# Optimization experiments

Measured on AMD Instinct MI355X. Metric: run time of the kernel, lower is better.

The kernel has to match this reference:

```python
import jax, jax.numpy as jnp
import numpy as np

B = 1_000_000   # reflections
K = 16_384      # groups
E = 64          # encoder_out
H = 64          # hidden_dim


def setup_inputs() -> dict:
    key = jax.random.key(0)
    ks = jax.random.split(key, 12)
    x = jax.random.normal(ks[0], (B, E), dtype=jnp.float32)
    gl = jax.random.randint(ks[1], (B,), 0, K)
    # guarantee every group id 0..K-1 appears, so torch.unique == arange(K)
    gl = gl.at[:K].set(jnp.arange(K))
    s = 0.05
    W1 = jax.random.normal(ks[2], (E, H), jnp.float32) * s
    b1 = jax.random.normal(ks[3], (H,), jnp.float32) * s
    W2 = jax.random.normal(ks[4], (H, H), jnp.float32) * s
    b2 = jax.random.normal(ks[5], (H,), jnp.float32) * s
    W3 = jax.random.normal(ks[6], (H, H), jnp.float32) * s
    b3 = jax.random.normal(ks[7], (H,), jnp.float32) * s
    w_mu = jax.random.normal(ks[8], (H, 1), jnp.float32) * s
    b_mu = jnp.full((1,), -6.9, jnp.float32)   # log_tau_init
    w_lv = jax.random.normal(ks[9], (H, 1), jnp.float32) * s
    b_lv = jnp.full((1,), -2.0, jnp.float32)
    return {"x": x, "group_labels": gl, "W1": W1, "b1": b1, "W2": W2, "b2": b2,
            "W3": W3, "b3": b3, "w_mu": w_mu, "b_mu": b_mu, "w_lv": w_lv, "b_lv": b_lv}


def reference(x, group_labels, W1, b1, W2, b2, W3, b3, w_mu, b_mu, w_lv, b_lv):
    # phi: Linear -> SiLU -> Linear -> SiLU
    z = jax.nn.silu(jax.nn.silu(x @ W1 + b1) @ W2 + b2)          # (B, H)
    # segment mean by group (math-equivalent to the dense one-hot matmul)
    counts = jax.ops.segment_sum(jnp.ones((z.shape[0],), z.dtype),
                                 group_labels, num_segments=K)    # (K,)
    gsum = jax.ops.segment_sum(z, group_labels, num_segments=K)   # (K, H)
    group_features = gsum / counts[:, None]
    # rho + heads
    h = jax.nn.silu(group_features @ W3 + b3)                     # (K, H)
    mu = (h @ w_mu + b_mu)[:, 0]                                  # (K,)
    logvar = jnp.clip((h @ w_lv + b_lv)[:, 0], -10.0, 4.0)        # (K,)
    std = jnp.exp(0.5 * logvar)
    eps = jax.random.normal(jax.random.key(42), std.shape, std.dtype)
    log_tau = mu + std * eps                                      # reparam sample
    tau_group = jnp.exp(log_tau)
    # unique_groups == arange(K) by construction -> searchsorted is identity
    tau_per_refl = tau_group[group_labels][:, None]               # (B, 1)
    log_tau_per_refl = log_tau[group_labels][:, None]             # (B, 1)
    return (mu, logvar, tau_per_refl, log_tau_per_refl)
```

## Files before the change

### kernel.cpp

```cpp
#include <hip/hip_runtime.h>

#define BN 1000000
#define KN 16384
#define HN 64
#define TPB 384
#define NW  6

typedef __bf16 bf16x8 __attribute__((ext_vector_type(8)));
typedef float  f32x4  __attribute__((ext_vector_type(4)));
typedef unsigned short u16x8 __attribute__((ext_vector_type(8)));

__device__ __forceinline__ unsigned short f2bf(float f) {
    unsigned u = __float_as_uint(f);
    u += 0x7fffu + ((u >> 16) & 1u);
    return (unsigned short)(u >> 16);
}
__device__ __forceinline__ float bf2f(unsigned short b) {
    return __uint_as_float(((unsigned)b) << 16);
}
__device__ __forceinline__ float silu_f(float v) {
    return v * __builtin_amdgcn_rcpf(1.0f + __expf(-v));
}
__device__ __forceinline__ f32x4 mfma16(bf16x8 a, bf16x8 b, f32x4 c) {
    return __builtin_amdgcn_mfma_f32_16x16x32_bf16(a, b, c, 0, 0, 0);
}

__device__ __forceinline__ float erfinv_xla(float x) {
    float w = -log1pf(-x * x);
    float p;
    if (w < 5.0f) {
        w -= 2.5f;
        p = 2.81022636e-08f;
        p = fmaf(p, w, 3.43273939e-07f);
        p = fmaf(p, w, -3.5233877e-06f);
        p = fmaf(p, w, -4.39150654e-06f);
        p = fmaf(p, w, 0.00021858087f);
        p = fmaf(p, w, -0.00125372503f);
        p = fmaf(p, w, -0.00417768164f);
        p = fmaf(p, w, 0.246640727f);
        p = fmaf(p, w, 1.50140941f);
    } else {
        w = sqrtf(w) - 3.0f;
        p = -0.000200214257f;
        p = fmaf(p, w, 0.000100950558f);
        p = fmaf(p, w, 0.00134934322f);
        p = fmaf(p, w, -0.00367342844f);
        p = fmaf(p, w, 0.00573950773f);
        p = fmaf(p, w, -0.0076224613f);
        p = fmaf(p, w, 0.00943887047f);
        p = fmaf(p, w, 1.00167406f);
        p = fmaf(p, w, 2.83297682f);
    }
    return p * x;
}

__device__ __forceinline__ float jax_eps16384(int gid) {
    const unsigned k0 = 0u, k1 = 42u, k2 = 0x1BD11BDAu ^ 0u ^ 42u;
    unsigned x0 = 0u + k0;
    unsigned x1 = (unsigned)gid + k1;
#define TF_RND(r) { x0 += x1; x1 = (x1 << (r)) | (x1 >> (32 - (r))); x1 ^= x0; }
    TF_RND(13) TF_RND(15) TF_RND(26) TF_RND(6)  x0 += k1; x1 += k2 + 1u;
    TF_RND(17) TF_RND(29) TF_RND(16) TF_RND(24) x0 += k2; x1 += k0 + 2u;
    TF_RND(13) TF_RND(15) TF_RND(26) TF_RND(6)  x0 += k0; x1 += k1 + 3u;
    TF_RND(17) TF_RND(29) TF_RND(16) TF_RND(24) x0 += k1; x1 += k2 + 4u;
    TF_RND(13) TF_RND(15) TF_RND(26) TF_RND(6)  x0 += k2; x1 += k0 + 5u;
#undef TF_RND
    unsigned bits = x0 ^ x1;
    float f = __uint_as_float((bits >> 9) | 0x3f800000u) - 1.0f;
    const float mn = -0.99999994f;
    float u = fmaxf(f * 2.0f + mn, mn);
    return 1.41421354f * erfinv_xla(u);
}

__global__ __launch_bounds__(256) void k_count(const int* __restrict__ gl,
                                               int* __restrict__ counts,
                                               float4* __restrict__ gz) {
    int i = blockIdx.x * 256 + threadIdx.x;
    const float4 z4 = make_float4(0.f, 0.f, 0.f, 0.f);
    for (int j = i; j < KN * HN / 4; j += 250112) gz[j] = z4;
    if (i < BN / 4) {
        int4 g = ((const int4*)gl)[i];
        atomicAdd(&counts[g.x], 1); atomicAdd(&counts[g.y], 1);
        atomicAdd(&counts[g.z], 1); atomicAdd(&counts[g.w], 1);
    }
}

__global__ __launch_bounds__(1024) void k_scan(const int* __restrict__ counts, int* __restrict__ cursor) {
    __shared__ int wtot[16];
    const int t = threadIdx.x, lane = t & 63, wv = t >> 6;
    const int4* c4 = (const int4*)counts;
    int4 q0 = c4[t * 4], q1 = c4[t * 4 + 1], q2 = c4[t * 4 + 2], q3 = c4[t * 4 + 3];
    int c[16] = {q0.x, q0.y, q0.z, q0.w, q1.x, q1.y, q1.z, q1.w,
                 q2.x, q2.y, q2.z, q2.w, q3.x, q3.y, q3.z, q3.w};
    int loc[16], s = 0;
    #pragma unroll
    for (int i = 0; i < 16; ++i) { loc[i] = s; s += c[i]; }
    const int own = s;
    #pragma unroll
    for (int off = 1; off < 64; off <<= 1) {
        int v = __shfl_up(s, off);
        if (lane >= off) s += v;
    }
    if (lane == 63) wtot[wv] = s;
    __syncthreads();
    int wbase = 0;
    #pragma unroll
    for (int w = 0; w < 16; ++w) wbase += (w < wv) ? wtot[w] : 0;
    const int ebase = wbase + s - own;
    int o[16];
    #pragma unroll
    for (int i = 0; i < 16; ++i) o[i] = ebase + loc[i];
    int4* o4 = (int4*)cursor;
    o4[t * 4]     = make_int4(o[0],  o[1],  o[2],  o[3]);
    o4[t * 4 + 1] = make_int4(o[4],  o[5],  o[6],  o[7]);
    o4[t * 4 + 2] = make_int4(o[8],  o[9],  o[10], o[11]);
    o4[t * 4 + 3] = make_int4(o[12], o[13], o[14], o[15]);
}

__global__ __launch_bounds__(256) void k_scatter(const int* __restrict__ gl, int* __restrict__ cursor,
                                                 int2* __restrict__ spk) {
    int i = blockIdx.x * 256 + threadIdx.x;
    if (i < BN / 4) {
        int4 g = ((const int4*)gl)[i];
        int r = i * 4;
        int p0 = atomicAdd(&cursor[g.x], 1); spk[p0] = make_int2(r,     g.x);
        int p1 = atomicAdd(&cursor[g.y], 1); spk[p1] = make_int2(r + 1, g.y);
        int p2 = atomicAdd(&cursor[g.z], 1); spk[p2] = make_int2(r + 2, g.z);
        int p3 = atomicAdd(&cursor[g.w], 1); spk[p3] = make_int2(r + 3, g.w);
    }
}

__global__ __launch_bounds__(TPB, 3) void k_phase1(
    const float* __restrict__ x, const int2* __restrict__ spk,
    const float* __restrict__ W1, const float* __restrict__ b1,
    const float* __restrict__ W2, const float* __restrict__ b2,
    float* __restrict__ gsum)
{
    __shared__ __align__(16) unsigned short w1t[64 * 64];
    __shared__ __align__(16) unsigned short w2t[64 * 64];
    __shared__ __align__(16) unsigned short xh[NW][64 * 64];
    __shared__ float b1s[64], b2s[64];
    __shared__ __align__(16) int sg_s[TPB];

    const int t = threadIdx.x;
    const int wv = t >> 6, lane = t & 63;
    const int lj = lane & 15, lg = lane >> 4;
    const int base  = blockIdx.x * TPB;
    const int wbase = base + wv * 64;

    const float4* W1v = (const float4*)W1;
    const float4* W2v = (const float4*)W2;
    float4 wa[3], wb[3];
    #pragma unroll
    for (int i = 0; i < 3; ++i) {
        int e4 = i * TPB + t;
        if (e4 < 1024) { wa[i] = W1v[e4]; wb[i] = W2v[e4]; }
    }

    int rid[4];
    #pragma unroll
    for (int rt = 0; rt < 4; ++rt) {
        int r = wbase + rt * 16 + lj;
        rid[rt] = (r < BN) ? spk[r].x : 0;
    }
    float4 xr[4][4];
    #pragma unroll
    for (int rt = 0; rt < 4; ++rt) {
        const float* xp = x + (size_t)rid[rt] * 64 + lg * 8;
        xr[rt][0] = *(const float4*)(xp);
        xr[rt][1] = *(const float4*)(xp + 4);
        xr[rt][2] = *(const float4*)(xp + 32);
        xr[rt][3] = *(const float4*)(xp + 36);
    }

    #pragma unroll
    for (int i = 0; i < 3; ++i) {
        int e4 = i * TPB + t;
        if (e4 < 1024) {
            int k  = e4 >> 4;
            int j0 = (e4 & 15) * 4;
            float av[4] = {wa[i].x, wa[i].y, wa[i].z, wa[i].w};
            float bv[4] = {wb[i].x, wb[i].y, wb[i].z, wb[i].w};
            #pragma unroll
            for (int c = 0; c < 4; ++c) {
                int j = j0 + c;
                int off = j * 128 + ((2 * k) ^ ((j & 7) << 4));
                *(unsigned short*)((char*)w1t + off) = f2bf(av[c]);
                *(unsigned short*)((char*)w2t + off) = f2bf(bv[c]);
            }
        }
    }
    if (t < 64) { b1s[t] = b1[t]; b2s[t] = b2[t]; }
    sg_s[t] = (base + t < BN) ? spk[base + t].y : -1;
    __syncthreads();

    bf16x8 af[4][2];
    #pragma unroll
    for (int rt = 0; rt < 4; ++rt)
        #pragma unroll
        for (int kk = 0; kk < 2; ++kk) {
            float4 a = xr[rt][kk * 2], b = xr[rt][kk * 2 + 1];
            u16x8 u;
            u[0] = f2bf(a.x); u[1] = f2bf(a.y); u[2] = f2bf(a.z); u[3] = f2bf(a.w);
            u[4] = f2bf(b.x); u[5] = f2bf(b.y); u[6] = f2bf(b.z); u[7] = f2bf(b.w);
            af[rt][kk] = __builtin_bit_cast(bf16x8, u);
        }

    unsigned short* myx = &xh[wv][0];

    f32x4 acc[4][4];
    #pragma unroll
    for (int a = 0; a < 4; ++a)
        #pragma unroll
        for (int b = 0; b < 4; ++b) acc[a][b] = f32x4{0.f, 0.f, 0.f, 0.f};

    #pragma unroll
    for (int kk = 0; kk < 2; ++kk) {
        const int kbyte = kk * 64 + lg * 16;
        bf16x8 bw[4];
        #pragma unroll
        for (int ct = 0; ct < 4; ++ct) {
            int row = ct * 16 + lj;
            bw[ct] = *(const bf16x8*)((char*)w1t + row * 128 + (kbyte ^ ((row & 7) << 4)));
        }
        #pragma unroll
        for (int rt = 0; rt < 4; ++rt)
            #pragma unroll
            for (int ct = 0; ct < 4; ++ct)
                acc[rt][ct] = mfma16(af[rt][kk], bw[ct], acc[rt][ct]);
    }
    {
        float bc[4];
        #pragma unroll
        for (int ct = 0; ct < 4; ++ct) bc[ct] = b1s[ct * 16 + lj];
        #pragma unroll
        for (int rt = 0; rt < 4; ++rt) {
            #pragma unroll
            for (int ct = 0; ct < 4; ++ct) {
                f32x4 v = acc[rt][ct];
                #pragma unroll
                for (int rg = 0; rg < 4; ++rg) {
                    int row = rt * 16 + lg * 4 + rg;
                    int col = ct * 16 + lj;
                    float h = silu_f(v[rg] + bc[ct]);
                    int off = row * 128 + ((2 * col) ^ ((row & 7) << 4));
                    *(unsigned short*)((char*)myx + off) = f2bf(h);
                }
                acc[rt][ct] = f32x4{0.f, 0.f, 0.f, 0.f};
            }
        }
    }

    #pragma unroll
    for (int kk = 0; kk < 2; ++kk) {
        const int kbyte = kk * 64 + lg * 16;
        bf16x8 bw[4];
        #pragma unroll
        for (int ct = 0; ct < 4; ++ct) {
            int row = ct * 16 + lj;
            bw[ct] = *(const bf16x8*)((char*)w2t + row * 128 + (kbyte ^ ((row & 7) << 4)));
        }
        #pragma unroll
        for (int rt = 0; rt < 4; ++rt) {
            int row = rt * 16 + lj;
            bf16x8 aw = *(const bf16x8*)((char*)myx + row * 128 + (kbyte ^ ((row & 7) << 4)));
            #pragma unroll
            for (int ct = 0; ct < 4; ++ct)
                acc[rt][ct] = mfma16(aw, bw[ct], acc[rt][ct]);
        }
    }
    {
        float bc[4];
        #pragma unroll
        for (int ct = 0; ct < 4; ++ct) bc[ct] = b2s[ct * 16 + lj];
        #pragma unroll
        for (int rt = 0; rt < 4; ++rt) {
            #pragma unroll
            for (int ct = 0; ct < 4; ++ct) {
                f32x4 v = acc[rt][ct];
                int col  = ct * 16 + lj;
                int row0 = rt * 16 + lg * 4;
                ushort4 pk;
                pk.x = f2bf(silu_f(v[0] + bc[ct]));
                pk.y = f2bf(silu_f(v[1] + bc[ct]));
                pk.z = f2bf(silu_f(v[2] + bc[ct]));
                pk.w = f2bf(silu_f(v[3] + bc[ct]));
                *(ushort4*)((char*)myx + col * 128 + ((2 * row0) ^ ((col & 7) << 4))) = pk;
            }
        }
    }

    {
        const int c  = lane;
        const char* zT = (const char*)myx;
        float vsum = 0.0f;
        int curg = -2;
        #pragma unroll
        for (int blk = 0; blk < 8; ++blk) {
            u16x8 v = *(const u16x8*)(zT + c * 128 + ((16 * blk) ^ ((c & 7) << 4)));
            int4 ga = *(const int4*)(&sg_s[wv * 64 + blk * 8]);
            int4 gb = *(const int4*)(&sg_s[wv * 64 + blk * 8 + 4]);
            int gs[8] = {ga.x, ga.y, ga.z, ga.w, gb.x, gb.y, gb.z, gb.w};
            #pragma unroll
            for (int j = 0; j < 8; ++j) {
                int g = gs[j];
                if (g != curg) {
                    if (curg >= 0) atomicAdd(&gsum[curg * 64 + c], vsum);
                    vsum = 0.0f;
                    curg = g;
                }
                vsum += bf2f(v[j]);
            }
        }
        if (curg >= 0) atomicAdd(&gsum[curg * 64 + c], vsum);
    }
}

__global__ __launch_bounds__(64) void k_phase2(
    const float* __restrict__ gsum, const int* __restrict__ counts,
    const float* __restrict__ W3, const float* __restrict__ b3,
    const float* __restrict__ wmu, const float* __restrict__ bmu,
    const float* __restrict__ wlv, const float* __restrict__ blv,
    float* __restrict__ out, float* __restrict__ taug, float* __restrict__ ltaug)
{
    __shared__ __align__(16) float w3t[64 * 64];
    __shared__ float b3s[64], wmus[64], wlvs[64];
    const int t = threadIdx.x;
    for (int i = 0; i < 64; ++i) w3t[t * 64 + i] = W3[i * 64 + t];
    b3s[t] = b3[t]; wmus[t] = wmu[t]; wlvs[t] = wlv[t];
    __syncthreads();

    const int gid = blockIdx.x * 64 + t;
    const float inv = 1.0f / (float)counts[gid];
    float gf[64];
    #pragma unroll
    for (int i = 0; i < 16; ++i) {
        float4 v = *(const float4*)(gsum + (size_t)gid * 64 + i * 4);
        gf[i * 4 + 0] = v.x * inv; gf[i * 4 + 1] = v.y * inv;
        gf[i * 4 + 2] = v.z * inv; gf[i * 4 + 3] = v.w * inv;
    }
    float mu = bmu[0], lv = blv[0];
    for (int j = 0; j < 64; ++j) {
        float a = b3s[j];
        const float4* wr = (const float4*)(w3t + j * 64);
        #pragma unroll
        for (int k = 0; k < 16; ++k) {
            float4 wv = wr[k];
            a += gf[k * 4 + 0] * wv.x + gf[k * 4 + 1] * wv.y
               + gf[k * 4 + 2] * wv.z + gf[k * 4 + 3] * wv.w;
        }
        float h = silu_f(a);
        mu += h * wmus[j];
        lv += h * wlvs[j];
    }
    lv = fminf(fmaxf(lv, -10.0f), 4.0f);
    float sd  = __expf(0.5f * lv);
    float eps = jax_eps16384(gid);
    float lt  = mu + sd * eps;
    out[gid]      = mu;
    out[KN + gid] = lv;
    taug[gid]  = __expf(lt);
    ltaug[gid] = lt;
}

__global__ __launch_bounds__(256) void k_phase3(
    const int* __restrict__ gl, const float* __restrict__ taug,
    const float* __restrict__ ltaug, float* __restrict__ out)
{
    int i = blockIdx.x * 256 + threadIdx.x;
    if (i < BN / 4) {
        int4 g = ((const int4*)gl)[i];
        float4 tv = make_float4(taug[g.x],  taug[g.y],  taug[g.z],  taug[g.w]);
        float4 lv = make_float4(ltaug[g.x], ltaug[g.y], ltaug[g.z], ltaug[g.w]);
        ((float4*)(out + 2 * KN))[i]      = tv;
        ((float4*)(out + 2 * KN + BN))[i] = lv;
    }
}

extern "C" void kernel_launch(void* const* d_in, const int* in_sizes, int n_in,
                              void* d_out, int out_size, void* d_ws, size_t ws_size,
                              hipStream_t stream)
{
    const float* x   = (const float*)d_in[0];
    const int*   gl  = (const int*)d_in[1];
    const float* W1  = (const float*)d_in[2];
    const float* b1  = (const float*)d_in[3];
    const float* W2  = (const float*)d_in[4];
    const float* b2  = (const float*)d_in[5];
    const float* W3  = (const float*)d_in[6];
    const float* b3  = (const float*)d_in[7];
    const float* wmu = (const float*)d_in[8];
    const float* bmu = (const float*)d_in[9];
    const float* wlv = (const float*)d_in[10];
    const float* blv = (const float*)d_in[11];
    float* out = (float*)d_out;

    float* ws     = (float*)d_ws;
    float* gsum   = ws;
    int*   counts = (int*)(gsum + KN * HN);
    int*   cursor = counts + KN;
    float* taug   = (float*)(cursor + KN);
    float* ltaug  = taug + KN;
    int2*  spk    = (int2*)(ltaug + KN);

    hipMemsetAsync(counts, 0, (size_t)KN * sizeof(int), stream);

    const int nb4 = (BN / 4 + 255) / 256;
    const int nb1 = (BN + TPB - 1) / TPB;
    k_count  <<<nb4, 256, 0, stream>>>(gl, counts, (float4*)gsum);
    k_scan   <<<1, 1024, 0, stream>>>(counts, cursor);
    k_scatter<<<nb4, 256, 0, stream>>>(gl, cursor, spk);
    k_phase1 <<<nb1, TPB, 0, stream>>>(x, spk, W1, b1, W2, b2, gsum);
    k_phase2 <<<KN / 64, 64, 0, stream>>>(gsum, counts, W3, b3, wmu, bmu, wlv, blv, out, taug, ltaug);
    k_phase3 <<<nb4, 256, 0, stream>>>(gl, taug, ltaug, out);
}
```

Measured before the change: 263.1 us.

## Make phase1 persistent with software-pipelined gather of sorted rows

Converts the MLP+segment-sum kernel into a persistent grid of 512 blocks of 256 threads that loop over 256-row chunks. The weights are converted and loaded into LDS once per block instead of once per chunk. The gather of the next chunk's x rows and the permutation indices two chunks ahead are prefetched into registers while the current chunk computes, to hide global-memory latency on the irregular gather. The cost is more register pressure from double-buffered x and index registers (launch bounds change to 2 blocks per SIMD), and fewer waves available for latency hiding.

```diff
diff --git a/kernel.cpp b/kernel.cpp
--- a/kernel.cpp
+++ b/kernel.cpp
@@ -3,8 +3,10 @@
 #define BN 1000000
 #define KN 16384
 #define HN 64
-#define TPB 384
-#define NW  6
+#define TPB 256
+#define NW  4
+#define NB  512
+#define NCHUNK ((BN + TPB - 1) / TPB)
 
 typedef __bf16 bf16x8 __attribute__((ext_vector_type(8)));
 typedef float  f32x4  __attribute__((ext_vector_type(4)));
@@ -130,7 +132,7 @@
     }
 }
 
-__global__ __launch_bounds__(TPB, 3) void k_phase1(
+__global__ __launch_bounds__(TPB, 2) void k_phase1(
     const float* __restrict__ x, const int2* __restrict__ spk,
     const float* __restrict__ W1, const float* __restrict__ b1,
     const float* __restrict__ W2, const float* __restrict__ b2,
@@ -140,47 +142,24 @@
     __shared__ __align__(16) unsigned short w2t[64 * 64];
     __shared__ __align__(16) unsigned short xh[NW][64 * 64];
     __shared__ float b1s[64], b2s[64];
-    __shared__ __align__(16) int sg_s[TPB];
+    __shared__ int sg_s[NW][64];
 
     const int t = threadIdx.x;
     const int wv = t >> 6, lane = t & 63;
     const int lj = lane & 15, lg = lane >> 4;
-    const int base  = blockIdx.x * TPB;
-    const int wbase = base + wv * 64;
-
-    const float4* W1v = (const float4*)W1;
-    const float4* W2v = (const float4*)W2;
-    float4 wa[3], wb[3];
-    #pragma unroll
-    for (int i = 0; i < 3; ++i) {
-        int e4 = i * TPB + t;
-        if (e4 < 1024) { wa[i] = W1v[e4]; wb[i] = W2v[e4]; }
-    }
-
-    int rid[4];
-    #pragma unroll
-    for (int rt = 0; rt < 4; ++rt) {
-        int r = wbase + rt * 16 + lj;
-        rid[rt] = (r < BN) ? spk[r].x : 0;
-    }
-    float4 xr[4][4];
-    #pragma unroll
-    for (int rt = 0; rt < 4; ++rt) {
-        const float* xp = x + (size_t)rid[rt] * 64 + lg * 8;
-        xr[rt][0] = *(const float4*)(xp);
-        xr[rt][1] = *(const float4*)(xp + 4);
-        xr[rt][2] = *(const float4*)(xp + 32);
-        xr[rt][3] = *(const float4*)(xp + 36);
-    }
-
-    #pragma unroll
-    for (int i = 0; i < 3; ++i) {
-        int e4 = i * TPB + t;
-        if (e4 < 1024) {
+
+    {
+        const float4* W1v = (const float4*)W1;
+        const float4* W2v = (const float4*)W2;
+        #pragma unroll
+        for (int i = 0; i < 4; ++i) {
+            int e4 = i * 256 + t;
             int k  = e4 >> 4;
             int j0 = (e4 & 15) * 4;
-            float av[4] = {wa[i].x, wa[i].y, wa[i].z, wa[i].w};
-            float bv[4] = {wb[i].x, wb[i].y, wb[i].z, wb[i].w};
+            float4 a = W1v[e4];
+            float4 b = W2v[e4];
+            float av[4] = {a.x, a.y, a.z, a.w};
+            float bv[4] = {b.x, b.y, b.z, b.w};
             #pragma unroll
             for (int c = 0; c < 4; ++c) {
                 int j = j0 + c;
@@ -189,50 +168,58 @@
                 *(unsigned short*)((char*)w2t + off) = f2bf(bv[c]);
             }
         }
-    }
-    if (t < 64) { b1s[t] = b1[t]; b2s[t] = b2[t]; }
-    sg_s[t] = (base + t < BN) ? spk[base + t].y : -1;
+        if (t < 64) { b1s[t] = b1[t]; b2s[t] = b2[t]; }
+    }
     __syncthreads();
 
+    float bc1[4], bc2[4];
+    #pragma unroll
+    for (int ct = 0; ct < 4; ++ct) { bc1[ct] = b1s[ct * 16 + lj]; bc2[ct] = b2s[ct * 16 + lj]; }
+
+    unsigned short* myx = &xh[wv][0];
+    int2   rsA[4], rsB[4];
+    float4 xr[4][4];
     bf16x8 af[4][2];
-    #pragma unroll
-    for (int rt = 0; rt < 4; ++rt)
+
+    auto load_spk = [&](int c, int2 (&dst)[4]) {
+        int cc = c < NCHUNK - 1 ? c : NCHUNK - 1;
+        #pragma unroll
+        for (int rt = 0; rt < 4; ++rt) {
+            int r = cc * TPB + wv * 64 + rt * 16 + lj;
+            dst[rt] = spk[r < BN ? r : BN - 1];
+        }
+    };
+    auto load_x = [&](const int2 (&src)[4]) {
+        #pragma unroll
+        for (int rt = 0; rt < 4; ++rt) {
+            const float* xp = x + (size_t)src[rt].x * 64 + lg * 8;
+            xr[rt][0] = *(const float4*)(xp);
+            xr[rt][1] = *(const float4*)(xp + 4);
+            xr[rt][2] = *(const float4*)(xp + 32);
+            xr[rt][3] = *(const float4*)(xp + 36);
+        }
+    };
+    auto compute = [&]() {
+        f32x4 acc[4][4];
+        #pragma unroll
+        for (int a = 0; a < 4; ++a)
+            #pragma unroll
+            for (int b = 0; b < 4; ++b) acc[a][b] = f32x4{0.f, 0.f, 0.f, 0.f};
         #pragma unroll
         for (int kk = 0; kk < 2; ++kk) {
-            float4 a = xr[rt][kk * 2], b = xr[rt][kk * 2 + 1];
-            u16x8 u;
-            u[0] = f2bf(a.x); u[1] = f2bf(a.y); u[2] = f2bf(a.z); u[3] = f2bf(a.w);
-            u[4] = f2bf(b.x); u[5] = f2bf(b.y); u[6] = f2bf(b.z); u[7] = f2bf(b.w);
-            af[rt][kk] = __builtin_bit_cast(bf16x8, u);
-        }
-
-    unsigned short* myx = &xh[wv][0];
-
-    f32x4 acc[4][4];
-    #pragma unroll
-    for (int a = 0; a < 4; ++a)
-        #pragma unroll
-        for (int b = 0; b < 4; ++b) acc[a][b] = f32x4{0.f, 0.f, 0.f, 0.f};
-
-    #pragma unroll
-    for (int kk = 0; kk < 2; ++kk) {
-        const int kbyte = kk * 64 + lg * 16;
-        bf16x8 bw[4];
-        #pragma unroll
-        for (int ct = 0; ct < 4; ++ct) {
-            int row = ct * 16 + lj;
-            bw[ct] = *(const bf16x8*)((char*)w1t + row * 128 + (kbyte ^ ((row & 7) << 4)));
-        }
-        #pragma unroll
-        for (int rt = 0; rt < 4; ++rt)
-            #pragma unroll
-            for (int ct = 0; ct < 4; ++ct)
-                acc[rt][ct] = mfma16(af[rt][kk], bw[ct], acc[rt][ct]);
-    }
-    {
-        float bc[4];
-        #pragma unroll
-        for (int ct = 0; ct < 4; ++ct) bc[ct] = b1s[ct * 16 + lj];
+            const int kbyte = kk * 64 + lg * 16;
+            bf16x8 bw[4];
+            #pragma unroll
+            for (int ct = 0; ct < 4; ++ct) {
+                int row = ct * 16 + lj;
+                bw[ct] = *(const bf16x8*)((char*)w1t + row * 128 + (kbyte ^ ((row & 7) << 4)));
+            }
+            #pragma unroll
+            for (int rt = 0; rt < 4; ++rt)
+                #pragma unroll
+                for (int ct = 0; ct < 4; ++ct)
+                    acc[rt][ct] = mfma16(af[rt][kk], bw[ct], acc[rt][ct]);
+        }
         #pragma unroll
         for (int rt = 0; rt < 4; ++rt) {
             #pragma unroll
@@ -242,37 +229,31 @@
                 for (int rg = 0; rg < 4; ++rg) {
                     int row = rt * 16 + lg * 4 + rg;
                     int col = ct * 16 + lj;
-                    float h = silu_f(v[rg] + bc[ct]);
+                    float h = silu_f(v[rg] + bc1[ct]);
                     int off = row * 128 + ((2 * col) ^ ((row & 7) << 4));
                     *(unsigned short*)((char*)myx + off) = f2bf(h);
                 }
                 acc[rt][ct] = f32x4{0.f, 0.f, 0.f, 0.f};
             }
         }
-    }
-
-    #pragma unroll
-    for (int kk = 0; kk < 2; ++kk) {
-        const int kbyte = kk * 64 + lg * 16;
-        bf16x8 bw[4];
-        #pragma unroll
-        for (int ct = 0; ct < 4; ++ct) {
-            int row = ct * 16 + lj;
-            bw[ct] = *(const bf16x8*)((char*)w2t + row * 128 + (kbyte ^ ((row & 7) << 4)));
-        }
-        #pragma unroll
-        for (int rt = 0; rt < 4; ++rt) {
-            int row = rt * 16 + lj;
-            bf16x8 aw = *(const bf16x8*)((char*)myx + row * 128 + (kbyte ^ ((row & 7) << 4)));
-            #pragma unroll
-            for (int ct = 0; ct < 4; ++ct)
-                acc[rt][ct] = mfma16(aw, bw[ct], acc[rt][ct]);
-        }
-    }
-    {
-        float bc[4];
-        #pragma unroll
-        for (int ct = 0; ct < 4; ++ct) bc[ct] = b2s[ct * 16 + lj];
+        #pragma unroll
+        for (int kk = 0; kk < 2; ++kk) {
+            const int kbyte = kk * 64 + lg * 16;
+            bf16x8 bw[4];
+            #pragma unroll
+            for (int ct = 0; ct < 4; ++ct) {
+                int row = ct * 16 + lj;
+                bw[ct] = *(const bf16x8*)((char*)w2t + row * 128 + (kbyte ^ ((row & 7) << 4)));
+            }
+            #pragma unroll
+            for (int rt = 0; rt < 4; ++rt) {
+                int row = rt * 16 + lj;
+                bf16x8 aw = *(const bf16x8*)((char*)myx + row * 128 + (kbyte ^ ((row & 7) << 4)));
+                #pragma unroll
+                for (int ct = 0; ct < 4; ++ct)
+                    acc[rt][ct] = mfma16(aw, bw[ct], acc[rt][ct]);
+            }
+        }
         #pragma unroll
         for (int rt = 0; rt < 4; ++rt) {
             #pragma unroll
@@ -281,38 +262,71 @@
                 int col  = ct * 16 + lj;
                 int row0 = rt * 16 + lg * 4;
                 ushort4 pk;
-                pk.x = f2bf(silu_f(v[0] + bc[ct]));
-                pk.y = f2bf(silu_f(v[1] + bc[ct]));
-                pk.z = f2bf(silu_f(v[2] + bc[ct]));
-                pk.w = f2bf(silu_f(v[3] + bc[ct]));
+                pk.x = f2bf(silu_f(v[0] + bc2[ct]));
+                pk.y = f2bf(silu_f(v[1] + bc2[ct]));
+                pk.z = f2bf(silu_f(v[2] + bc2[ct]));
+                pk.w = f2bf(silu_f(v[3] + bc2[ct]));
                 *(ushort4*)((char*)myx + col * 128 + ((2 * row0) ^ ((col & 7) << 4))) = pk;
             }
         }
-    }
-
-    {
-        const int c  = lane;
-        const char* zT = (const char*)myx;
-        float vsum = 0.0f;
-        int curg = -2;
-        #pragma unroll
-        for (int blk = 0; blk < 8; ++blk) {
-            u16x8 v = *(const u16x8*)(zT + c * 128 + ((16 * blk) ^ ((c & 7) << 4)));
-            int4 ga = *(const int4*)(&sg_s[wv * 64 + blk * 8]);
-            int4 gb = *(const int4*)(&sg_s[wv * 64 + blk * 8 + 4]);
-            int gs[8] = {ga.x, ga.y, ga.z, ga.w, gb.x, gb.y, gb.z, gb.w};
-            #pragma unroll
-            for (int j = 0; j < 8; ++j) {
-                int g = gs[j];
-                if (g != curg) {
-                    if (curg >= 0) atomicAdd(&gsum[curg * 64 + c], vsum);
-                    vsum = 0.0f;
-                    curg = g;
+        {
+            const int c = lane;
+            const char* zT = (const char*)myx;
+            float vsum = 0.0f;
+            int curg = -2;
+            #pragma unroll
+            for (int blk = 0; blk < 8; ++blk) {
+                u16x8 v = *(const u16x8*)(zT + c * 128 + ((16 * blk) ^ ((c & 7) << 4)));
+                int4 ga = *(const int4*)(&sg_s[wv][blk * 8]);
+                int4 gb = *(const int4*)(&sg_s[wv][blk * 8 + 4]);
+                int gs[8] = {ga.x, ga.y, ga.z, ga.w, gb.x, gb.y, gb.z, gb.w};
+                #pragma unroll
+                for (int j = 0; j < 8; ++j) {
+                    int g = gs[j];
+                    if (g != curg) {
+                        if (curg >= 0) atomicAdd(&gsum[curg * 64 + c], vsum);
+                        vsum = 0.0f;
+                        curg = g;
+                    }
+                    vsum += bf2f(v[j]);
                 }
-                vsum += bf2f(v[j]);
-            }
-        }
-        if (curg >= 0) atomicAdd(&gsum[curg * 64 + c], vsum);
+            }
+            if (curg >= 0) atomicAdd(&gsum[curg * 64 + c], vsum);
+        }
+    };
+
+    auto pstep = [&](int2 (&CUR)[4], int2 (&NXT)[4], int c) {
+        if (lg == 0) {
+            #pragma unroll
+            for (int rt = 0; rt < 4; ++rt) {
+                int r = c * TPB + wv * 64 + rt * 16 + lj;
+                sg_s[wv][rt * 16 + lj] = (r < BN) ? CUR[rt].y : -1;
+            }
+        }
+        #pragma unroll
+        for (int rt = 0; rt < 4; ++rt)
+            #pragma unroll
+            for (int kk = 0; kk < 2; ++kk) {
+                float4 a = xr[rt][kk * 2], b = xr[rt][kk * 2 + 1];
+                u16x8 u;
+                u[0] = f2bf(a.x); u[1] = f2bf(a.y); u[2] = f2bf(a.z); u[3] = f2bf(a.w);
+                u[4] = f2bf(b.x); u[5] = f2bf(b.y); u[6] = f2bf(b.z); u[7] = f2bf(b.w);
+                af[rt][kk] = __builtin_bit_cast(bf16x8, u);
+            }
+        load_x(NXT);
+        load_spk(c + 2 * NB, CUR);
+        compute();
+    };
+
+    const int c0 = blockIdx.x;
+    load_spk(c0, rsA);
+    load_spk(c0 + NB, rsB);
+    load_x(rsA);
+
+    int c = c0;
+    while (true) {
+        pstep(rsA, rsB, c); c += NB; if (c >= NCHUNK) break;
+        pstep(rsB, rsA, c); c += NB; if (c >= NCHUNK) break;
     }
 }
 
@@ -406,11 +420,10 @@
     hipMemsetAsync(counts, 0, (size_t)KN * sizeof(int), stream);
 
     const int nb4 = (BN / 4 + 255) / 256;
-    const int nb1 = (BN + TPB - 1) / TPB;
     k_count  <<<nb4, 256, 0, stream>>>(gl, counts, (float4*)gsum);
     k_scan   <<<1, 1024, 0, stream>>>(counts, cursor);
     k_scatter<<<nb4, 256, 0, stream>>>(gl, cursor, spk);
-    k_phase1 <<<nb1, TPB, 0, stream>>>(x, spk, W1, b1, W2, b2, gsum);
+    k_phase1 <<<NB, TPB, 0, stream>>>(x, spk, W1, b1, W2, b2, gsum);
     k_phase2 <<<KN / 64, 64, 0, stream>>>(gsum, counts, W3, b3, wmu, bmu, wlv, blv, out, taug, ltaug);
     k_phase3 <<<nb4, 256, 0, stream>>>(gl, taug, ltaug, out);
 }
```

Result: faster. 250.1 us (-4.9%).
